# Optimization experiments

Hardware: AMD Instinct MI355X
Metric: run time of the kernel (lower is better)

## Reference

```python
import jax, jax.numpy as jnp
import numpy as np

NUM_HEADS = 16


def setup_inputs() -> dict:
    key = jax.random.key(0)
    ks = jax.random.split(key, 9)
    B, S, C = 2, 2048, 1024
    s = 1.0 / np.sqrt(C)
    return {
        "hidden_states": jax.random.normal(ks[0], (B, S, C), jnp.float32),
        "Wq": jax.random.normal(ks[1], (C, C), jnp.float32) * s,
        "bq": jnp.zeros((C,), jnp.float32),
        "Wk": jax.random.normal(ks[2], (C, C), jnp.float32) * s,
        "bk": jnp.zeros((C,), jnp.float32),
        "Wv": jax.random.normal(ks[3], (C, C), jnp.float32) * s,
        "bv": jnp.zeros((C,), jnp.float32),
        "Wo": jax.random.normal(ks[4], (C, C), jnp.float32) * s,
        "bo": jnp.zeros((C,), jnp.float32),
    }


def reference(hidden_states, Wq, bq, Wk, bk, Wv, bv, Wo, bo):
    # Self-attention path of AttnProcessor (3D input, no mask, no norms,
    # residual_connection=True, rescale_output_factor=1.0).
    B, S, C = hidden_states.shape
    H = NUM_HEADS
    D = C // H
    residual = hidden_states

    q = hidden_states @ Wq + bq  # [B,S,C]
    k = hidden_states @ Wk + bk
    v = hidden_states @ Wv + bv

    # head_to_batch_dim: [B,S,C] -> [B,S,H,D]
    q = q.reshape(B, S, H, D)
    k = k.reshape(B, S, H, D)
    v = v.reshape(B, S, H, D)

    scale = 1.0 / np.sqrt(D).astype(np.float32)
    # get_attention_scores: baddbmm with scale, then softmax (full [B,H,S,S])
    scores = jnp.einsum("bqhd,bkhd->bhqk", q, k) * scale
    probs = jax.nn.softmax(scores, axis=-1)

    out = jnp.einsum("bhqk,bkhd->bqhd", probs, v)  # bmm(probs, value)
    out = out.reshape(B, S, C)  # batch_to_head_dim

    out = out @ Wo + bo  # to_out[0]; to_out[1] is dropout (identity in eval)
    out = out + residual  # residual_connection
    return out  # rescale_output_factor = 1.0
```

## Files before the change

### kernel.cpp

```cpp
#include <hip/hip_runtime.h>

#define BATCH 2
#define SEQ   2048
#define CH    1024
#define NHEAD 16
#define HDIM  64
#define MROWS (BATCH * SEQ)

typedef __attribute__((ext_vector_type(8))) short short8;
typedef __attribute__((ext_vector_type(4))) float floatx4;
typedef unsigned short ushort_t;

__device__ __forceinline__ float b2f(ushort_t u) {
    union { unsigned int i; float f; } x;
    x.i = ((unsigned int)u) << 16;
    return x.f;
}
__device__ __forceinline__ ushort_t f2b(float f) {
    union { float f; unsigned int i; } x;
    x.f = f;
    unsigned int lsb = (x.i >> 16) & 1u;
    x.i += 0x7fffu + lsb;
    return (ushort_t)(x.i >> 16);
}
__device__ __forceinline__ unsigned pack2(float a, float b) {
    return (unsigned)f2b(a) | ((unsigned)f2b(b) << 16);
}
__device__ __forceinline__ unsigned cvt_pk_bf16(float a, float b) {
    unsigned r;
    asm("v_cvt_pk_bf16_f32 %0, %1, %2" : "=v"(r) : "v"(a), "v"(b));
    return r;
}

__device__ __forceinline__ void gld16(const ushort_t* g, ushort_t* l) {
    __builtin_amdgcn_global_load_lds(
        (const __attribute__((address_space(1))) void*)g,
        (__attribute__((address_space(3))) void*)l, 16, 0, 0);
}

template <int VM>
__device__ __forceinline__ void vm_barrier() {
    asm volatile("s_waitcnt vmcnt(%0)\n\ts_barrier" ::"i"(VM) : "memory");
}

__global__ __launch_bounds__(256) void cvt_bf16_kernel(
    const float* __restrict__ in, ushort_t* __restrict__ out, int n4) {
    int i = blockIdx.x * blockDim.x + threadIdx.x;
    if (i < n4) {
        float4 v = ((const float4*)in)[i];
        ushort4 o = {f2b(v.x), f2b(v.y), f2b(v.z), f2b(v.w)};
        ((ushort4*)out)[i] = o;
    }
}

__global__ __launch_bounds__(256) void transpose_cvt_all(
    const float* __restrict__ W0, const float* __restrict__ W1,
    const float* __restrict__ W2, const float* __restrict__ W3,
    ushort_t* __restrict__ T0, ushort_t* __restrict__ T1,
    ushort_t* __restrict__ T2, ushort_t* __restrict__ T3) {
    __shared__ ushort_t T[64][68];
    const int z = blockIdx.z;
    const float* W = (z == 0) ? W0 : (z == 1) ? W1 : (z == 2) ? W2 : W3;
    ushort_t* Wt = (z == 0) ? T0 : (z == 1) ? T1 : (z == 2) ? T2 : T3;
    const int tid = threadIdx.x;
    const int n0 = blockIdx.x * 64, k0 = blockIdx.y * 64;
    const int r = tid >> 4, c4 = (tid & 15) * 4;
#pragma unroll
    for (int p = 0; p < 4; p++) {
        int k = p * 16 + r;
        float4 v = *(const float4*)&W[(size_t)(k0 + k) * CH + n0 + c4];
        T[c4 + 0][k] = f2b(v.x);
        T[c4 + 1][k] = f2b(v.y);
        T[c4 + 2][k] = f2b(v.z);
        T[c4 + 3][k] = f2b(v.w);
    }
    __syncthreads();
#pragma unroll
    for (int p = 0; p < 4; p++) {
        int n = p * 16 + r;
        ushort4 o = {T[n][c4 + 0], T[n][c4 + 1], T[n][c4 + 2], T[n][c4 + 3]};
        *(ushort4*)&Wt[(size_t)(n0 + n) * CH + k0 + c4] = o;
    }
}

__device__ __forceinline__ void gemm_core_db(
    const ushort_t* __restrict__ A, const ushort_t* __restrict__ Bt,
    int bm, int n0, int tid, floatx4 acc[4][4], ushort_t* lds) {
    const int wave = tid >> 6, lane = tid & 63;
    const int quad = lane >> 4, t16 = lane & 15;
    const int wm = wave >> 1, wn = wave & 1;
    const int arow = tid >> 2, ak = (tid & 3) * 8;

    const ushort_t* a0 = A + (size_t)(bm + arow) * CH + ak;
    const ushort_t* a1 = A + (size_t)(bm + 64 + arow) * CH + ak;
    const ushort_t* b0 = Bt + (size_t)(n0 + arow) * CH + ak;
    const ushort_t* b1 = Bt + (size_t)(n0 + 64 + arow) * CH + ak;

#pragma unroll
    for (int i = 0; i < 4; i++)
#pragma unroll
        for (int j = 0; j < 4; j++) acc[i][j] = (floatx4){0.f, 0.f, 0.f, 0.f};

    auto stage = [&](int k, ushort_t* buf) {
        gld16(a0 + k, buf + wave * 512);
        gld16(a1 + k, buf + 2048 + wave * 512);
        gld16(b0 + k, buf + 4096 + wave * 512);
        gld16(b1 + k, buf + 6144 + wave * 512);
    };
    auto compute = [&](const ushort_t* As) {
        const ushort_t* Bs = As + 4096;
        short8 af[4], bf[4];
#pragma unroll
        for (int i = 0; i < 4; i++)
            af[i] = *(const short8*)&As[(wm * 64 + i * 16 + t16) * 32 + quad * 8];
#pragma unroll
        for (int j = 0; j < 4; j++)
            bf[j] = *(const short8*)&Bs[(wn * 64 + j * 16 + t16) * 32 + quad * 8];
#pragma unroll
        for (int i = 0; i < 4; i++)
#pragma unroll
            for (int j = 0; j < 4; j++)
                acc[i][j] = __builtin_amdgcn_mfma_f32_16x16x32_bf16(
                    af[i], bf[j], acc[i][j], 0, 0, 0);
    };

    ushort_t* bcur = lds;
    ushort_t* bnext = lds + 8192;
    ushort_t* bfar = lds + 16384;

    stage(0, bcur);
    stage(32, bnext);

    for (int it = 0; it < CH / 32 - 2; ++it) {
        stage((it + 2) * 32, bfar);
        vm_barrier<8>();
        compute(bcur);
        ushort_t* t = bcur; bcur = bnext; bnext = bfar; bfar = t;
    }
    vm_barrier<4>();
    compute(bcur);
    vm_barrier<0>();
    compute(bnext);
}

__global__ __launch_bounds__(256) void gemm_qkv(
    const ushort_t* __restrict__ X,
    const ushort_t* __restrict__ WqT, const ushort_t* __restrict__ WkT,
    const ushort_t* __restrict__ WvT,
    const float* __restrict__ bq, const float* __restrict__ bk,
    const float* __restrict__ bv,
    ushort_t* __restrict__ Qm, ushort_t* __restrict__ Km,
    ushort_t* __restrict__ Vtm) {
    __shared__ ushort_t lds[3 * 8192];
    const int tid = threadIdx.x;
    const int seg = blockIdx.x >> 3;
    const int n0 = (blockIdx.x & 7) * 128;
    const int bm = blockIdx.y * 128;
    const ushort_t* Bt = (seg == 0) ? WqT : (seg == 1) ? WkT : WvT;
    const float* bias = (seg == 0) ? bq : (seg == 1) ? bk : bv;

    floatx4 acc[4][4];
    gemm_core_db(X, Bt, bm, n0, tid, acc, lds);

    const int lane = tid & 63, wave = tid >> 6;
    const int quad = lane >> 4, t16 = lane & 15;
    const int wm = wave >> 1, wn = wave & 1;

    if (seg < 2) {
        ushort_t* outp = seg ? Km : Qm;
        const float sc = seg ? 1.0f : 0.125f;
#pragma unroll
        for (int i = 0; i < 4; i++)
#pragma unroll
            for (int j = 0; j < 4; j++) {
                const int col = n0 + wn * 64 + j * 16 + t16;
                const float bb = bias[col];
                const int row0 = bm + wm * 64 + i * 16 + quad * 4;
#pragma unroll
                for (int r = 0; r < 4; r++)
                    outp[(size_t)(row0 + r) * CH + col] =
                        f2b((acc[i][j][r] + bb) * sc);
            }
    } else {
        ushort_t* rep = lds;
        const int b = bm >> 11;
        const int s_base = bm & (SEQ - 1);
#pragma unroll
        for (int half = 0; half < 2; half++) {
            __syncthreads();
            if (wn == half) {
#pragma unroll
                for (int i = 0; i < 4; i++)
#pragma unroll
                    for (int j = 0; j < 4; j++) {
                        const int dl = j * 16 + t16;
                        const int sl = wm * 64 + i * 16 + quad * 4;
                        const float bb = bias[n0 + half * 64 + dl];
                        uint2 w = {pack2(acc[i][j][0] + bb, acc[i][j][1] + bb),
                                   pack2(acc[i][j][2] + bb, acc[i][j][3] + bb)};
                        *(uint2*)&rep[dl * 136 + sl] = w;
                    }
            }
            __syncthreads();
#pragma unroll
            for (int step = 0; step < 4; step++) {
                const int dl = step * 16 + (tid >> 4);
                const int sl = (tid & 15) * 8;
                short8 v = *(const short8*)&rep[dl * 136 + sl];
                const int col = n0 + half * 64 + dl;
                const int h = col >> 6, dd = col & 63;
                *(short8*)&Vtm[(((size_t)b * NHEAD + h) * HDIM + dd) * SEQ +
                               s_base + sl] = v;
            }
        }
    }
}

__global__ __launch_bounds__(256) void gemm_out(
    const ushort_t* __restrict__ Am, const ushort_t* __restrict__ WoT,
    const float* __restrict__ bo, const float* __restrict__ resid,
    float* __restrict__ out) {
    __shared__ ushort_t lds[3 * 6144];
    const int tid = threadIdx.x;
    const int n0 = blockIdx.x * 64;
    const int bm = blockIdx.y * 128;
    const int wave = tid >> 6, lane = tid & 63;
    const int quad = lane >> 4, t16 = lane & 15;
    const int arow = tid >> 2, ak = (tid & 3) * 8;

    const ushort_t* a0 = Am + (size_t)(bm + arow) * CH + ak;
    const ushort_t* a1 = Am + (size_t)(bm + 64 + arow) * CH + ak;
    const ushort_t* b0 = WoT + (size_t)(n0 + arow) * CH + ak;

    floatx4 acc[2][4];
#pragma unroll
    for (int i = 0; i < 2; i++)
#pragma unroll
        for (int j = 0; j < 4; j++) acc[i][j] = (floatx4){0.f, 0.f, 0.f, 0.f};

    auto stage = [&](int k, ushort_t* buf) {
        gld16(a0 + k, buf + wave * 512);
        gld16(a1 + k, buf + 2048 + wave * 512);
        gld16(b0 + k, buf + 4096 + wave * 512);
    };
    auto compute = [&](const ushort_t* As) {
        const ushort_t* Bs = As + 4096;
        short8 af[2], bf[4];
#pragma unroll
        for (int i = 0; i < 2; i++)
            af[i] = *(const short8*)&As[(wave * 32 + i * 16 + t16) * 32 + quad * 8];
#pragma unroll
        for (int j = 0; j < 4; j++)
            bf[j] = *(const short8*)&Bs[(j * 16 + t16) * 32 + quad * 8];
#pragma unroll
        for (int i = 0; i < 2; i++)
#pragma unroll
            for (int j = 0; j < 4; j++)
                acc[i][j] = __builtin_amdgcn_mfma_f32_16x16x32_bf16(
                    af[i], bf[j], acc[i][j], 0, 0, 0);
    };

    ushort_t* bcur = lds;
    ushort_t* bnext = lds + 6144;
    ushort_t* bfar = lds + 12288;

    stage(0, bcur);
    stage(32, bnext);

    for (int it = 0; it < CH / 32 - 2; ++it) {
        stage((it + 2) * 32, bfar);
        vm_barrier<6>();
        compute(bcur);
        ushort_t* t = bcur; bcur = bnext; bnext = bfar; bfar = t;
    }
    vm_barrier<3>();
    compute(bcur);
    vm_barrier<0>();
    compute(bnext);

#pragma unroll
    for (int i = 0; i < 2; i++)
#pragma unroll
        for (int j = 0; j < 4; j++) {
            const int col = n0 + j * 16 + t16;
            const float bb = bo[col];
            const int row0 = bm + wave * 32 + i * 16 + quad * 4;
#pragma unroll
            for (int r = 0; r < 4; r++) {
                const size_t idx = (size_t)(row0 + r) * CH + col;
                out[idx] = acc[i][j][r] + bb + resid[idx];
            }
        }
}

__global__ __launch_bounds__(512, 4) void flash_attn_mfma(
    const ushort_t* __restrict__ Q, const ushort_t* __restrict__ K,
    const ushort_t* __restrict__ Vt, ushort_t* __restrict__ O) {
    __shared__ ushort_t Ks[64][72];
    __shared__ ushort_t Vs[64][72];

    const int tid = threadIdx.x;
    const int wave = tid >> 6, lane = tid & 63;
    const int quad = lane >> 4, t16 = lane & 15;
    const int bh = blockIdx.y, b = bh >> 4, h = bh & 15;
    const int q0 = blockIdx.x * 128;

    const size_t base_q = ((size_t)b * SEQ) * CH + (size_t)h * HDIM;
    const size_t base_vt = ((size_t)(b * NHEAD + h)) * HDIM * SEQ;

    short8 qf[2];
    {
        const ushort_t* qp =
            Q + base_q + (size_t)(q0 + wave * 16 + t16) * CH + quad * 8;
        qf[0] = *(const short8*)(qp);
        qf[1] = *(const short8*)(qp + 32);
    }

    const short8 ones = (short8)(short)0x3F80;

    floatx4 Oa[4];
    floatx4 Oe = (floatx4){0.f, 0.f, 0.f, 0.f};
#pragma unroll
    for (int d = 0; d < 4; d++) Oa[d] = (floatx4){0.f, 0.f, 0.f, 0.f};

    const int r4 = tid >> 3;
    const int t8 = tid & 7;
    const int c8 = t8 * 8;
    const ushort_t* kp = K + base_q + (size_t)r4 * CH + c8;
    const ushort_t* vp = Vt + base_vt + (size_t)r4 * SEQ + c8;

    const int vcol0 = ((t8 & 4) << 3) + (((2 * t8) & 3) << 3) + (((t8 >> 1) & 1) << 2);
    const int vcol1 = ((t8 & 4) << 3) + (((2 * t8 + 1) & 3) << 3) + (((t8 >> 1) & 1) << 2);

    short8 kreg = *(const short8*)(kp);
    short8 vreg = *(const short8*)(vp);

    for (int k0 = 0; k0 < SEQ; k0 += 64) {
        __syncthreads();
        *(short8*)&Ks[r4][c8] = kreg;
        {
            union { short8 s; uint4 u; } vv; vv.s = vreg;
            *(uint2*)&Vs[r4][vcol0] = (uint2){vv.u.x, vv.u.y};
            *(uint2*)&Vs[r4][vcol1] = (uint2){vv.u.z, vv.u.w};
        }
        __syncthreads();
        if (k0 + 64 < SEQ) {
            kreg = *(const short8*)(kp + (size_t)(k0 + 64) * CH);
            vreg = *(const short8*)(vp + (k0 + 64));
        }

        uint2 pw[4];
#pragma unroll
        for (int j = 0; j < 4; j++) {
            short8 kf0 = *(const short8*)(&Ks[j * 16 + t16][quad * 8]);
            short8 kf1 = *(const short8*)(&Ks[j * 16 + t16][32 + quad * 8]);
            floatx4 z = (floatx4){0.f, 0.f, 0.f, 0.f};
            z = __builtin_amdgcn_mfma_f32_16x16x32_bf16(kf0, qf[0], z, 0, 0, 0);
            z = __builtin_amdgcn_mfma_f32_16x16x32_bf16(kf1, qf[1], z, 0, 0, 0);
            pw[j].x = cvt_pk_bf16(__expf(z[0]), __expf(z[1]));
            pw[j].y = cvt_pk_bf16(__expf(z[2]), __expf(z[3]));
        }
        short8 pf0, pf1;
        {
            union { uint4 u; short8 s; } c0, c1;
            c0.u = (uint4){pw[0].x, pw[0].y, pw[1].x, pw[1].y};
            c1.u = (uint4){pw[2].x, pw[2].y, pw[3].x, pw[3].y};
            pf0 = c0.s;
            pf1 = c1.s;
        }

        __builtin_amdgcn_s_setprio(1);
#pragma unroll
        for (int d = 0; d < 4; d++) {
            short8 vf0 = *(const short8*)(&Vs[d * 16 + t16][quad * 8]);
            short8 vf1 = *(const short8*)(&Vs[d * 16 + t16][32 + quad * 8]);
            Oa[d] = __builtin_amdgcn_mfma_f32_16x16x32_bf16(pf0, vf0, Oa[d], 0, 0, 0);
            Oa[d] = __builtin_amdgcn_mfma_f32_16x16x32_bf16(pf1, vf1, Oa[d], 0, 0, 0);
        }
        Oe = __builtin_amdgcn_mfma_f32_16x16x32_bf16(pf0, ones, Oe, 0, 0, 0);
        Oe = __builtin_amdgcn_mfma_f32_16x16x32_bf16(pf1, ones, Oe, 0, 0, 0);
        __builtin_amdgcn_s_setprio(0);
    }

    float inv[4];
#pragma unroll
    for (int r = 0; r < 4; r++) inv[r] = 1.f / Oe[r];
#pragma unroll
    for (int d = 0; d < 4; d++)
#pragma unroll
        for (int r = 0; r < 4; r++) {
            const int row = q0 + wave * 16 + quad * 4 + r;
            O[base_q + (size_t)row * CH + d * 16 + t16] =
                f2b(Oa[d][r] * inv[r]);
        }
}

extern "C" void kernel_launch(void* const* d_in, const int* in_sizes, int n_in,
                              void* d_out, int out_size, void* d_ws,
                              size_t ws_size, hipStream_t stream) {
    const float* X  = (const float*)d_in[0];
    const float* Wq = (const float*)d_in[1];
    const float* bq = (const float*)d_in[2];
    const float* Wk = (const float*)d_in[3];
    const float* bk = (const float*)d_in[4];
    const float* Wv = (const float*)d_in[5];
    const float* bv = (const float*)d_in[6];
    const float* Wo = (const float*)d_in[7];
    const float* bo = (const float*)d_in[8];
    float* out = (float*)d_out;

    const size_t MC = (size_t)MROWS * CH;
    const size_t WC = (size_t)CH * CH;
    ushort_t* ws  = (ushort_t*)d_ws;
    ushort_t* X16 = ws;
    ushort_t* Am  = ws;
    ushort_t* Qm  = ws + MC;
    ushort_t* Km  = ws + 2 * MC;
    ushort_t* Vtm = ws + 3 * MC;
    ushort_t* WqT = ws + 4 * MC;
    ushort_t* WkT = ws + 4 * MC + WC;
    ushort_t* WvT = ws + 4 * MC + 2 * WC;
    ushort_t* WoT = ws + 4 * MC + 3 * WC;

    dim3 blk(256);

    cvt_bf16_kernel<<<dim3((MC / 4 + 255) / 256), blk, 0, stream>>>(X, X16, (int)(MC / 4));
    transpose_cvt_all<<<dim3(16, 16, 4), blk, 0, stream>>>(
        Wq, Wk, Wv, Wo, WqT, WkT, WvT, WoT);

    gemm_qkv<<<dim3(24, 32), blk, 0, stream>>>(X16, WqT, WkT, WvT, bq, bk, bv,
                                               Qm, Km, Vtm);

    flash_attn_mfma<<<dim3(SEQ / 128, BATCH * NHEAD), dim3(512), 0, stream>>>(
        Qm, Km, Vtm, Am);

    gemm_out<<<dim3(16, 32), blk, 0, stream>>>(Am, WoT, bo, X, out);
}
```

Measured before the change: 188.0 us.

## Give each attention wave two query tiles and issue GEMM prefetch after barrier

The flash attention kernel drops from 512 to 256 threads per block, and each wave now handles 32 query rows (two 16-row tiles) instead of 16. Every K/V fragment read from LDS therefore feeds twice as many MFMAs, and each thread stages two K and two V vectors per tile. In both GEMMs the wait on outstanding memory loads now happens before the next stage is issued rather than after, so fewer loads are in flight while waiting. The cost is higher register pressure and fewer waves per block for hiding latency.

Result: no change. 187.1 us (-0.5%).

```diff
diff --git a/kernel.cpp b/kernel.cpp
--- a/kernel.cpp
+++ b/kernel.cpp
@@ -132,8 +132,8 @@
     stage(32, bnext);
 
     for (int it = 0; it < CH / 32 - 2; ++it) {
+        vm_barrier<4>();
         stage((it + 2) * 32, bfar);
-        vm_barrier<8>();
         compute(bcur);
         ushort_t* t = bcur; bcur = bnext; bnext = bfar; bfar = t;
     }
@@ -268,8 +268,8 @@
     stage(32, bnext);
 
     for (int it = 0; it < CH / 32 - 2; ++it) {
+        vm_barrier<3>();
         stage((it + 2) * 32, bfar);
-        vm_barrier<6>();
         compute(bcur);
         ushort_t* t = bcur; bcur = bnext; bnext = bfar; bfar = t;
     }
@@ -293,7 +293,7 @@
         }
 }
 
-__global__ __launch_bounds__(512, 4) void flash_attn_mfma(
+__global__ __launch_bounds__(256, 4) void flash_attn_mfma(
     const ushort_t* __restrict__ Q, const ushort_t* __restrict__ K,
     const ushort_t* __restrict__ Vt, ushort_t* __restrict__ O) {
     __shared__ ushort_t Ks[64][72];
@@ -308,65 +308,85 @@
     const size_t base_q = ((size_t)b * SEQ) * CH + (size_t)h * HDIM;
     const size_t base_vt = ((size_t)(b * NHEAD + h)) * HDIM * SEQ;
 
-    short8 qf[2];
-    {
+    short8 qf[2][2];
+#pragma unroll
+    for (int u = 0; u < 2; u++) {
         const ushort_t* qp =
-            Q + base_q + (size_t)(q0 + wave * 16 + t16) * CH + quad * 8;
-        qf[0] = *(const short8*)(qp);
-        qf[1] = *(const short8*)(qp + 32);
+            Q + base_q + (size_t)(q0 + wave * 32 + u * 16 + t16) * CH + quad * 8;
+        qf[u][0] = *(const short8*)(qp);
+        qf[u][1] = *(const short8*)(qp + 32);
     }
 
     const short8 ones = (short8)(short)0x3F80;
 
-    floatx4 Oa[4];
-    floatx4 Oe = (floatx4){0.f, 0.f, 0.f, 0.f};
-#pragma unroll
-    for (int d = 0; d < 4; d++) Oa[d] = (floatx4){0.f, 0.f, 0.f, 0.f};
-
-    const int r4 = tid >> 3;
-    const int t8 = tid & 7;
-    const int c8 = t8 * 8;
-    const ushort_t* kp = K + base_q + (size_t)r4 * CH + c8;
-    const ushort_t* vp = Vt + base_vt + (size_t)r4 * SEQ + c8;
-
-    const int vcol0 = ((t8 & 4) << 3) + (((2 * t8) & 3) << 3) + (((t8 >> 1) & 1) << 2);
-    const int vcol1 = ((t8 & 4) << 3) + (((2 * t8 + 1) & 3) << 3) + (((t8 >> 1) & 1) << 2);
-
-    short8 kreg = *(const short8*)(kp);
-    short8 vreg = *(const short8*)(vp);
+    floatx4 Oa[2][4];
+    floatx4 Oe[2];
+#pragma unroll
+    for (int u = 0; u < 2; u++) {
+        Oe[u] = (floatx4){0.f, 0.f, 0.f, 0.f};
+#pragma unroll
+        for (int d = 0; d < 4; d++) Oa[u][d] = (floatx4){0.f, 0.f, 0.f, 0.f};
+    }
+
+    const int r4 = tid >> 2;
+    const int t4 = tid & 3;
+    const ushort_t* kp = K + base_q + (size_t)r4 * CH + t4 * 8;
+    const ushort_t* vp = Vt + base_vt + (size_t)r4 * SEQ + t4 * 8;
+
+    const int c0 = t4, c1 = t4 + 4;
+    const int v00 = ((c0 & 4) << 3) + (((2 * c0) & 3) << 3) + (((c0 >> 1) & 1) << 2);
+    const int v01 = ((c0 & 4) << 3) + (((2 * c0 + 1) & 3) << 3) + (((c0 >> 1) & 1) << 2);
+    const int v10 = ((c1 & 4) << 3) + (((2 * c1) & 3) << 3) + (((c1 >> 1) & 1) << 2);
+    const int v11 = ((c1 & 4) << 3) + (((2 * c1 + 1) & 3) << 3) + (((c1 >> 1) & 1) << 2);
+
+    short8 kr0 = *(const short8*)(kp);
+    short8 kr1 = *(const short8*)(kp + 32);
+    short8 vr0 = *(const short8*)(vp);
+    short8 vr1 = *(const short8*)(vp + 32);
 
     for (int k0 = 0; k0 < SEQ; k0 += 64) {
         __syncthreads();
-        *(short8*)&Ks[r4][c8] = kreg;
+        *(short8*)&Ks[r4][t4 * 8] = kr0;
+        *(short8*)&Ks[r4][t4 * 8 + 32] = kr1;
         {
-            union { short8 s; uint4 u; } vv; vv.s = vreg;
-            *(uint2*)&Vs[r4][vcol0] = (uint2){vv.u.x, vv.u.y};
-            *(uint2*)&Vs[r4][vcol1] = (uint2){vv.u.z, vv.u.w};
+            union { short8 s; uint4 u; } va, vb;
+            va.s = vr0; vb.s = vr1;
+            *(uint2*)&Vs[r4][v00] = (uint2){va.u.x, va.u.y};
+            *(uint2*)&Vs[r4][v01] = (uint2){va.u.z, va.u.w};
+            *(uint2*)&Vs[r4][v10] = (uint2){vb.u.x, vb.u.y};
+            *(uint2*)&Vs[r4][v11] = (uint2){vb.u.z, vb.u.w};
         }
         __syncthreads();
         if (k0 + 64 < SEQ) {
-            kreg = *(const short8*)(kp + (size_t)(k0 + 64) * CH);
-            vreg = *(const short8*)(vp + (k0 + 64));
-        }
-
-        uint2 pw[4];
+            const ushort_t* nkp = kp + (size_t)(k0 + 64) * CH;
+            kr0 = *(const short8*)(nkp);
+            kr1 = *(const short8*)(nkp + 32);
+            vr0 = *(const short8*)(vp + (k0 + 64));
+            vr1 = *(const short8*)(vp + (k0 + 64) + 32);
+        }
+
+        unsigned pk[2][8];
 #pragma unroll
         for (int j = 0; j < 4; j++) {
             short8 kf0 = *(const short8*)(&Ks[j * 16 + t16][quad * 8]);
             short8 kf1 = *(const short8*)(&Ks[j * 16 + t16][32 + quad * 8]);
-            floatx4 z = (floatx4){0.f, 0.f, 0.f, 0.f};
-            z = __builtin_amdgcn_mfma_f32_16x16x32_bf16(kf0, qf[0], z, 0, 0, 0);
-            z = __builtin_amdgcn_mfma_f32_16x16x32_bf16(kf1, qf[1], z, 0, 0, 0);
-            pw[j].x = cvt_pk_bf16(__expf(z[0]), __expf(z[1]));
-            pw[j].y = cvt_pk_bf16(__expf(z[2]), __expf(z[3]));
-        }
-        short8 pf0, pf1;
-        {
-            union { uint4 u; short8 s; } c0, c1;
-            c0.u = (uint4){pw[0].x, pw[0].y, pw[1].x, pw[1].y};
-            c1.u = (uint4){pw[2].x, pw[2].y, pw[3].x, pw[3].y};
-            pf0 = c0.s;
-            pf1 = c1.s;
+#pragma unroll
+            for (int u = 0; u < 2; u++) {
+                floatx4 z = (floatx4){0.f, 0.f, 0.f, 0.f};
+                z = __builtin_amdgcn_mfma_f32_16x16x32_bf16(kf0, qf[u][0], z, 0, 0, 0);
+                z = __builtin_amdgcn_mfma_f32_16x16x32_bf16(kf1, qf[u][1], z, 0, 0, 0);
+                pk[u][j * 2] = cvt_pk_bf16(__expf(z[0]), __expf(z[1]));
+                pk[u][j * 2 + 1] = cvt_pk_bf16(__expf(z[2]), __expf(z[3]));
+            }
+        }
+        short8 pf[2][2];
+#pragma unroll
+        for (int u = 0; u < 2; u++) {
+            union { uint4 q; short8 s; } cc;
+            cc.q = (uint4){pk[u][0], pk[u][1], pk[u][2], pk[u][3]};
+            pf[u][0] = cc.s;
+            cc.q = (uint4){pk[u][4], pk[u][5], pk[u][6], pk[u][7]};
+            pf[u][1] = cc.s;
         }
 
         __builtin_amdgcn_s_setprio(1);
@@ -374,25 +394,34 @@
         for (int d = 0; d < 4; d++) {
             short8 vf0 = *(const short8*)(&Vs[d * 16 + t16][quad * 8]);
             short8 vf1 = *(const short8*)(&Vs[d * 16 + t16][32 + quad * 8]);
-            Oa[d] = __builtin_amdgcn_mfma_f32_16x16x32_bf16(pf0, vf0, Oa[d], 0, 0, 0);
-            Oa[d] = __builtin_amdgcn_mfma_f32_16x16x32_bf16(pf1, vf1, Oa[d], 0, 0, 0);
-        }
-        Oe = __builtin_amdgcn_mfma_f32_16x16x32_bf16(pf0, ones, Oe, 0, 0, 0);
-        Oe = __builtin_amdgcn_mfma_f32_16x16x32_bf16(pf1, ones, Oe, 0, 0, 0);
+#pragma unroll
+            for (int u = 0; u < 2; u++) {
+                Oa[u][d] = __builtin_amdgcn_mfma_f32_16x16x32_bf16(pf[u][0], vf0, Oa[u][d], 0, 0, 0);
+                Oa[u][d] = __builtin_amdgcn_mfma_f32_16x16x32_bf16(pf[u][1], vf1, Oa[u][d], 0, 0, 0);
+            }
+        }
+#pragma unroll
+        for (int u = 0; u < 2; u++) {
+            Oe[u] = __builtin_amdgcn_mfma_f32_16x16x32_bf16(pf[u][0], ones, Oe[u], 0, 0, 0);
+            Oe[u] = __builtin_amdgcn_mfma_f32_16x16x32_bf16(pf[u][1], ones, Oe[u], 0, 0, 0);
+        }
         __builtin_amdgcn_s_setprio(0);
     }
 
-    float inv[4];
-#pragma unroll
-    for (int r = 0; r < 4; r++) inv[r] = 1.f / Oe[r];
-#pragma unroll
-    for (int d = 0; d < 4; d++)
-#pragma unroll
-        for (int r = 0; r < 4; r++) {
-            const int row = q0 + wave * 16 + quad * 4 + r;
-            O[base_q + (size_t)row * CH + d * 16 + t16] =
-                f2b(Oa[d][r] * inv[r]);
-        }
+#pragma unroll
+    for (int u = 0; u < 2; u++) {
+        float inv[4];
+#pragma unroll
+        for (int r = 0; r < 4; r++) inv[r] = 1.f / Oe[u][r];
+#pragma unroll
+        for (int d = 0; d < 4; d++)
+#pragma unroll
+            for (int r = 0; r < 4; r++) {
+                const int row = q0 + wave * 32 + u * 16 + quad * 4 + r;
+                O[base_q + (size_t)row * CH + d * 16 + t16] =
+                    f2b(Oa[u][d][r] * inv[r]);
+            }
+    }
 }
 
 extern "C" void kernel_launch(void* const* d_in, const int* in_sizes, int n_in,
@@ -431,7 +460,7 @@
     gemm_qkv<<<dim3(24, 32), blk, 0, stream>>>(X16, WqT, WkT, WvT, bq, bk, bv,
                                                Qm, Km, Vtm);
 
-    flash_attn_mfma<<<dim3(SEQ / 128, BATCH * NHEAD), dim3(512), 0, stream>>>(
+    flash_attn_mfma<<<dim3(SEQ / 128, BATCH * NHEAD), blk, 0, stream>>>(
         Qm, Km, Vtm, Am);
 
     gemm_out<<<dim3(16, 32), blk, 0, stream>>>(Am, WoT, bo, X, out);
```
